# Kernel optimization log

Hardware: AMD Instinct MI355X
Metric: run time of the kernel (lower is better)

## Reference

```python
import jax, jax.numpy as jnp
import numpy as np


def conv1x1(x, w, b):
    # x: [B,Cin,H,W], w: [Cout,Cin], b: [Cout]
    return jnp.einsum('bchw,oc->bohw', x, w) + b[None, :, None, None]


def _lin_idx_w(in_size, out_size):
    # PyTorch bilinear, align_corners=False: src = max((i+0.5)*scale - 0.5, 0)
    scale = in_size / out_size
    src = jnp.maximum((jnp.arange(out_size, dtype=jnp.float32) + 0.5) * scale - 0.5, 0.0)
    i0 = jnp.floor(src).astype(jnp.int32)
    i0 = jnp.minimum(i0, in_size - 1)
    i1 = jnp.minimum(i0 + 1, in_size - 1)
    w1 = src - i0.astype(jnp.float32)
    return i0, i1, w1


def bilinear_resize(x, out_h, out_w):
    Hin, Win = x.shape[-2], x.shape[-1]
    y0, y1, wy = _lin_idx_w(Hin, out_h)
    x0, x1, wx = _lin_idx_w(Win, out_w)
    wy = wy[:, None]  # [out_h,1]
    rows = x[:, :, y0, :] * (1.0 - wy) + x[:, :, y1, :] * wy
    out = rows[:, :, :, x0] * (1.0 - wx) + rows[:, :, :, x1] * wx      # [B,C,out_h,out_w]
    return out


def setup_inputs() -> dict:
    key = jax.random.key(0)
    ks = jax.random.split(key, 10)
    C, C8 = 512, 64
    s = 1.0 / np.sqrt(C)
    return {
        'content': jax.random.normal(ks[0], (4, C, 64, 64), jnp.float32),
        'style': jax.random.normal(ks[1], (4, C, 80, 80), jnp.float32),
        'f_w': jax.random.normal(ks[2], (C8, C), jnp.float32) * s,
        'f_b': jax.random.normal(ks[3], (C8,), jnp.float32) * 0.01,
        'g_w': jax.random.normal(ks[4], (C8, C), jnp.float32) * s,
        'g_b': jax.random.normal(ks[5], (C8,), jnp.float32) * 0.01,
        'h_w': jax.random.normal(ks[6], (C, C), jnp.float32) * s,
        'h_b': jax.random.normal(ks[7], (C,), jnp.float32) * 0.01,
        'out_w': jax.random.normal(ks[8], (C, C), jnp.float32) * s,
        'out_b': jax.random.normal(ks[9], (C,), jnp.float32) * 0.01,
    }


def reference(content, style, f_w, f_b, g_w, g_b, h_w, h_b, out_w, out_b):
    B, C, H, W = content.shape
    HW = H * W
    f = conv1x1(content, f_w, f_b).reshape(B, -1, HW)                       # [B,C8,HW] (query, pre-transpose)
    g = bilinear_resize(conv1x1(style, g_w, g_b), H, W).reshape(B, -1, HW)  # [B,C8,HW]
    h = bilinear_resize(conv1x1(style, h_w, h_b), H, W).reshape(B, C, HW)   # [B,C,HW]
    attn = jax.nn.softmax(jnp.einsum('bcm,bcn->bmn', f, g), axis=-1)        # [B,HW_q,HW_k]
    out = jnp.einsum('bcn,bmn->bcm', h, attn).reshape(B, C, H, W)
    return conv1x1(out, out_w, out_b)
```

## Files before the change

### kernel.cpp

```cpp
#include <hip/hip_runtime.h>

#define NB 4
#define NC 512
#define ND 64
#define HW 4096
#define SPIN 6400

typedef _Float16 f16;
typedef _Float16 f16x8 __attribute__((ext_vector_type(8)));
typedef short s16x8 __attribute__((ext_vector_type(8)));
typedef float f32x4 __attribute__((ext_vector_type(4)));

__device__ __forceinline__ unsigned short f32_to_bf16(float x) {
  union { float f; unsigned u; } v; v.f = x;
  unsigned r = v.u + 0x7FFFu + ((v.u >> 16) & 1u);
  return (unsigned short)(r >> 16);
}

__device__ __forceinline__ void stv(float* p, float v) { *p = v; }
__device__ __forceinline__ void stv(f16* p, float v) { *p = (f16)v; }
__device__ __forceinline__ void stv(unsigned short* p, float v) { *p = f32_to_bf16(v); }

__global__ __launch_bounds__(256) void cvt_kernel(const float* __restrict__ in,
                                                  f16* __restrict__ out, int n) {
  int i = blockIdx.x * 256 + threadIdx.x;
  if (i < n) out[i] = (f16)in[i];
}

__global__ __launch_bounds__(256) void tcvt_kernel(const float* __restrict__ in,
                                                   f16* __restrict__ out) {
  __shared__ float Xs[64][65];
  int p0 = blockIdx.x * 64, c0 = blockIdx.y * 64, b = blockIdx.z;
  int t = threadIdx.x;
  const float* ib = in + ((size_t)b * NC + c0) * HW + p0;
  int pl = t & 63, cg = t >> 6;
#pragma unroll
  for (int k = 0; k < 16; ++k) {
    int c = cg * 16 + k;
    Xs[c][pl] = ib[(size_t)c * HW + pl];
  }
  __syncthreads();
  int p = t >> 2, cb = (t & 3) * 16;
  union { f16 h[16]; float4 q[2]; } u;
#pragma unroll
  for (int j = 0; j < 16; ++j) u.h[j] = (f16)Xs[cb + j][p];
  f16* ob = out + ((size_t)b * HW + p0 + p) * NC + c0 + cb;
  *(float4*)(ob) = u.q[0];
  *(float4*)(ob + 8) = u.q[1];
}

__global__ __launch_bounds__(256) void rstcvt_kernel(const float* __restrict__ X,
                                                     f16* __restrict__ Y) {
  __shared__ float Xs[64 * 165];
  int oy = blockIdx.x, c0 = blockIdx.y * 64, b = blockIdx.z;
  float syf = fmaxf((oy + 0.5f) * 1.25f - 0.5f, 0.f);
  int y0 = (int)syf; int y1 = min(y0 + 1, 79); float wy = syf - (float)y0;
  int t = threadIdx.x;
  const float* Xb = X + ((size_t)b * NC + c0) * SPIN;
#pragma unroll
  for (int k = 0; k < 10; ++k) {
    int idx = t + k * 256;
    int c = idx / 40;
    int rem = idx - c * 40;
    int yy = rem / 20;
    int x4 = rem - yy * 20;
    int ysrc = yy ? y1 : y0;
    float4 v = *(const float4*)(Xb + (size_t)c * SPIN + ysrc * 80 + x4 * 4);
    float* d = Xs + c * 165 + yy * 82 + x4 * 4;
    d[0] = v.x; d[1] = v.y; d[2] = v.z; d[3] = v.w;
  }
  __syncthreads();
  int ox = t >> 2, cb = (t & 3) * 16;
  float sxf = fmaxf((ox + 0.5f) * 1.25f - 0.5f, 0.f);
  int x0 = (int)sxf; int x1 = min(x0 + 1, 79); float wx = sxf - (float)x0;
  union { f16 h[16]; float4 q[2]; } u;
#pragma unroll
  for (int j = 0; j < 16; ++j) {
    const float* base = Xs + (cb + j) * 165;
    float a0 = base[x0], a1 = base[x1];
    float b0 = base[82 + x0], b1 = base[82 + x1];
    float r0 = a0 + (a1 - a0) * wx;
    float r1 = b0 + (b1 - b0) * wx;
    u.h[j] = (f16)(r0 + (r1 - r0) * wy);
  }
  f16* ob = Y + ((size_t)b * HW + oy * 64 + ox) * NC + c0 + cb;
  *(float4*)(ob) = u.q[0];
  *(float4*)(ob + 8) = u.q[1];
}

__global__ __launch_bounds__(256) void convpm_kernel(const f16* __restrict__ X,
                                                     const f16* __restrict__ W,
                                                     const float* __restrict__ bias,
                                                     f16* __restrict__ Y) {
  int b = blockIdx.z;
  int t = threadIdx.x, l = t & 63, w = t >> 6;
  int pw = blockIdx.x * 256 + w * 64;
  int l4 = l & 15, g = l >> 4;
  f32x4 acc[4][4] = {};
  const f16* Xb = X + ((size_t)b * HW + pw) * NC;
  for (int kk = 0; kk < 16; ++kk) {
    int co = kk * 32 + g * 8;
    f16x8 a[4], bb[4];
#pragma unroll
    for (int ms = 0; ms < 4; ++ms) a[ms] = *(const f16x8*)(Xb + (size_t)(ms * 16 + l4) * NC + co);
#pragma unroll
    for (int ct = 0; ct < 4; ++ct) bb[ct] = *(const f16x8*)(W + (size_t)(ct * 16 + l4) * NC + co);
#pragma unroll
    for (int ms = 0; ms < 4; ++ms)
#pragma unroll
      for (int ct = 0; ct < 4; ++ct)
        acc[ms][ct] = __builtin_amdgcn_mfma_f32_16x16x32_f16(a[ms], bb[ct], acc[ms][ct], 0, 0, 0);
  }
  float bv[4];
#pragma unroll
  for (int ct = 0; ct < 4; ++ct) bv[ct] = bias[ct * 16 + l4];
  f16* Yb = Y + ((size_t)b * HW + pw) * ND;
#pragma unroll
  for (int ms = 0; ms < 4; ++ms)
#pragma unroll
    for (int ct = 0; ct < 4; ++ct)
#pragma unroll
      for (int r = 0; r < 4; ++r)
        Yb[(size_t)(ms * 16 + g * 4 + r) * ND + ct * 16 + l4] = (f16)(acc[ms][ct][r] + bv[ct]);
}

template <typename OUT_T>
__global__ __launch_bounds__(256) void convcm_kernel(const f16* __restrict__ X,
                                                     const f16* __restrict__ W,
                                                     const float* __restrict__ bias,
                                                     OUT_T* __restrict__ Y, int O) {
  int b = blockIdx.z;
  int o0 = blockIdx.x * 64;
  int t = threadIdx.x, l = t & 63, w = t >> 6;
  int pw = blockIdx.y * 256 + w * 64;
  int l4 = l & 15, g = l >> 4;
  f32x4 acc[4][4] = {};
  const f16* Xb = X + ((size_t)b * HW + pw) * NC;
  const f16* Wb = W + (size_t)o0 * NC;
  for (int kk = 0; kk < 16; ++kk) {
    int co = kk * 32 + g * 8;
    f16x8 a[4], bb[4];
#pragma unroll
    for (int ms = 0; ms < 4; ++ms) a[ms] = *(const f16x8*)(Wb + (size_t)(ms * 16 + l4) * NC + co);
#pragma unroll
    for (int ct = 0; ct < 4; ++ct) bb[ct] = *(const f16x8*)(Xb + (size_t)(ct * 16 + l4) * NC + co);
#pragma unroll
    for (int ms = 0; ms < 4; ++ms)
#pragma unroll
      for (int ct = 0; ct < 4; ++ct)
        acc[ms][ct] = __builtin_amdgcn_mfma_f32_16x16x32_f16(a[ms], bb[ct], acc[ms][ct], 0, 0, 0);
  }
  float bv[4][4];
#pragma unroll
  for (int ms = 0; ms < 4; ++ms)
#pragma unroll
    for (int r = 0; r < 4; ++r) bv[ms][r] = bias[o0 + ms * 16 + g * 4 + r];
#pragma unroll
  for (int ms = 0; ms < 4; ++ms)
#pragma unroll
    for (int ct = 0; ct < 4; ++ct)
#pragma unroll
      for (int r = 0; r < 4; ++r) {
        float val = acc[ms][ct][r] + bv[ms][r];
        stv(&Y[((size_t)b * O + o0 + ms * 16 + g * 4 + r) * HW + pw + ct * 16 + l4], val);
      }
}

__global__ __launch_bounds__(512, 4) void attn_kernel(const f16* __restrict__ FT,
                                                      const f16* __restrict__ GT,
                                                      const unsigned short* __restrict__ HC,
                                                      f16* __restrict__ MIDT) {
  __shared__ __align__(16) char KsB[128 * 128];
  __shared__ __align__(16) char PsB[64 * 256];
  __shared__ float denP[8][16];
  int bid = blockIdx.x;
  int b = (bid & 7) >> 1;
  int cs = bid & 1;
  int m0 = (bid >> 3) * 64;
  int t = threadIdx.x, l = t & 63, w = t >> 6;
  int l4 = l & 15, g = l >> 4;
  int msq = w >> 1;
  int nsq = (w & 1) * 4;

  const f16* Fb = FT + ((size_t)b * HW + m0 + msq * 16 + l4) * ND + g * 8;
  f16x8 qa0 = *(const f16x8*)(Fb);
  f16x8 qa1 = *(const f16x8*)(Fb + 32);

  f32x4 acc[4][2] = {};
  float den_acc[4] = {0.f, 0.f, 0.f, 0.f};

  const f16* Gb = GT + (size_t)b * HW * ND;
  const unsigned short* Hb = HC + ((size_t)b * NC + cs * 256 + w * 32) * HW;

  for (int n0 = 0; n0 < HW; n0 += 128) {
    __syncthreads();
#pragma unroll
    for (int i = 0; i < 2; ++i) {
      int idx = t + i * 512;
      int nl = idx >> 3, cc = idx & 7;
      f16x8 kv = *(const f16x8*)(Gb + (size_t)(n0 + nl) * ND + cc * 8);
      *(f16x8*)(KsB + ((nl * 128 + cc * 16) ^ ((nl & 7) << 4))) = kv;
    }
    __syncthreads();
    float dp[4] = {0.f, 0.f, 0.f, 0.f};
#pragma unroll
    for (int f = 0; f < 4; ++f) {
      int n = (nsq + f) * 16 + l4;
      int sw = (n & 7) << 4;
      f16x8 kb0 = *(const f16x8*)(KsB + ((n * 128 + g * 16) ^ sw));
      f16x8 kb1 = *(const f16x8*)(KsB + ((n * 128 + 64 + g * 16) ^ sw));
      f32x4 s = {};
      s = __builtin_amdgcn_mfma_f32_16x16x32_f16(qa0, kb0, s, 0, 0, 0);
      s = __builtin_amdgcn_mfma_f32_16x16x32_f16(qa1, kb1, s, 0, 0, 0);
#pragma unroll
      for (int r = 0; r < 4; ++r) {
        float p = __expf(s[r]);
        dp[r] += p;
        int row = msq * 16 + g * 4 + r;
        *(unsigned short*)(PsB + ((row * 256 + n * 2) ^ ((row & 7) << 4))) = f32_to_bf16(p);
      }
    }
#pragma unroll
    for (int r = 0; r < 4; ++r) {
      float v = dp[r];
      v += __shfl_xor(v, 1); v += __shfl_xor(v, 2);
      v += __shfl_xor(v, 4); v += __shfl_xor(v, 8);
      den_acc[r] += v;
    }
    __syncthreads();
#pragma unroll
    for (int khh = 0; khh < 2; ++khh) {
      s16x8 pa[4][2];
#pragma unroll
      for (int ms = 0; ms < 4; ++ms) {
        int row = ms * 16 + l4;
        int sw = (row & 7) << 4;
        pa[ms][0] = *(const s16x8*)(PsB + ((row * 256 + khh * 128 + g * 16) ^ sw));
        pa[ms][1] = *(const s16x8*)(PsB + ((row * 256 + khh * 128 + 64 + g * 16) ^ sw));
      }
#pragma unroll
      for (int ct = 0; ct < 2; ++ct) {
        const unsigned short* hp = Hb + (size_t)(ct * 16 + l4) * HW + n0 + khh * 64 + g * 8;
        s16x8 vb0 = *(const s16x8*)(hp);
        s16x8 vb1 = *(const s16x8*)(hp + 32);
#pragma unroll
        for (int ms = 0; ms < 4; ++ms) {
          acc[ms][ct] = __builtin_amdgcn_mfma_f32_16x16x32_bf16(pa[ms][0], vb0, acc[ms][ct], 0, 0, 0);
          acc[ms][ct] = __builtin_amdgcn_mfma_f32_16x16x32_bf16(pa[ms][1], vb1, acc[ms][ct], 0, 0, 0);
        }
      }
    }
  }
  if (l4 == 0) {
#pragma unroll
    for (int r = 0; r < 4; ++r) denP[w][g * 4 + r] = den_acc[r];
  }
  __syncthreads();
  f16* Mb = MIDT + ((size_t)b * HW + m0) * NC + cs * 256 + w * 32;
#pragma unroll
  for (int ms = 0; ms < 4; ++ms)
#pragma unroll
    for (int r = 0; r < 4; ++r) {
      float rd = 1.f / (denP[2 * ms][g * 4 + r] + denP[2 * ms + 1][g * 4 + r]);
#pragma unroll
      for (int ct = 0; ct < 2; ++ct)
        Mb[(size_t)(ms * 16 + g * 4 + r) * NC + ct * 16 + l4] = (f16)(acc[ms][ct][r] * rd);
    }
}

extern "C" void kernel_launch(void* const* d_in, const int* in_sizes, int n_in,
                              void* d_out, int out_size, void* d_ws, size_t ws_size,
                              hipStream_t stream) {
  const float* content = (const float*)d_in[0];
  const float* style   = (const float*)d_in[1];
  const float* f_w = (const float*)d_in[2];
  const float* f_b = (const float*)d_in[3];
  const float* g_w = (const float*)d_in[4];
  const float* g_b = (const float*)d_in[5];
  const float* h_w = (const float*)d_in[6];
  const float* h_b = (const float*)d_in[7];
  const float* out_w = (const float*)d_in[8];
  const float* out_b = (const float*)d_in[9];
  float* out = (float*)d_out;

  const size_t MB = 1ull << 20;
  char* base = (char*)d_ws;
  f16* contentT = (f16*)base;
  f16* midT     = (f16*)base;
  unsigned short* hC = (unsigned short*)(base + 16 * MB);
  f16* fT = (f16*)(base + 32 * MB);
  f16* gT = (f16*)(base + 34 * MB);
  f16* styrT = (f16*)(base + 48 * MB);
  f16* fw16 = (f16*)(base + 64 * MB);
  f16* gw16 = fw16 + ND * NC;
  f16* hw16 = gw16 + ND * NC;
  f16* ow16 = hw16 + NC * NC;

  cvt_kernel<<<dim3((ND * NC + 255) / 256), 256, 0, stream>>>(f_w, fw16, ND * NC);
  cvt_kernel<<<dim3((ND * NC + 255) / 256), 256, 0, stream>>>(g_w, gw16, ND * NC);
  cvt_kernel<<<dim3((NC * NC + 255) / 256), 256, 0, stream>>>(h_w, hw16, NC * NC);
  cvt_kernel<<<dim3((NC * NC + 255) / 256), 256, 0, stream>>>(out_w, ow16, NC * NC);
  tcvt_kernel<<<dim3(HW / 64, NC / 64, NB), 256, 0, stream>>>(content, contentT);
  rstcvt_kernel<<<dim3(64, NC / 64, NB), 256, 0, stream>>>(style, styrT);
  convpm_kernel<<<dim3(HW / 256, 1, NB), 256, 0, stream>>>(contentT, fw16, f_b, fT);
  convpm_kernel<<<dim3(HW / 256, 1, NB), 256, 0, stream>>>(styrT, gw16, g_b, gT);
  convcm_kernel<unsigned short><<<dim3(NC / 64, HW / 256, NB), 256, 0, stream>>>(styrT, hw16, h_b, hC, NC);
  attn_kernel<<<dim3(512), 512, 0, stream>>>(fT, gT, hC, midT);
  convcm_kernel<float><<<dim3(NC / 64, HW / 256, NB), 256, 0, stream>>>(midT, ow16, out_b, out, NC);
}
```

Before: 318.1 us.

## Double-buffer key tiles in attention and merge small conversion/projection launches

The attention kernel now double-buffers the key tile in shared memory, prefetching the next tile into registers while computing the current one. It issues the V (h) global loads early, raises wave priority around the MFMA bursts and defers the denominator shuffle-reduction to after the loop. Separately, the four weight conversion launches are merged into one kernel and the f/g projections into one launch, cutting launch overhead. The changes add shared memory and register pressure in the attention kernel, which may lower occupancy.

```diff
diff --git a/kernel.cpp b/kernel.cpp
--- a/kernel.cpp
+++ b/kernel.cpp
@@ -21,10 +21,18 @@
 __device__ __forceinline__ void stv(f16* p, float v) { *p = (f16)v; }
 __device__ __forceinline__ void stv(unsigned short* p, float v) { *p = f32_to_bf16(v); }
 
-__global__ __launch_bounds__(256) void cvt_kernel(const float* __restrict__ in,
-                                                  f16* __restrict__ out, int n) {
+__global__ __launch_bounds__(256) void cvtw_kernel(const float* __restrict__ fw,
+                                                   const float* __restrict__ gw,
+                                                   const float* __restrict__ hw,
+                                                   const float* __restrict__ ow,
+                                                   f16* __restrict__ dst) {
   int i = blockIdx.x * 256 + threadIdx.x;
-  if (i < n) out[i] = (f16)in[i];
+  const float* src; int off;
+  if (i < 32768) { src = fw; off = 0; }
+  else if (i < 65536) { src = gw; off = 32768; }
+  else if (i < 327680) { src = hw; off = 65536; }
+  else { src = ow; off = 327680; }
+  dst[i] = (f16)src[i - off];
 }
 
 __global__ __launch_bounds__(256) void tcvt_kernel(const float* __restrict__ in,
@@ -88,11 +96,19 @@
   *(float4*)(ob + 8) = u.q[1];
 }
 
-__global__ __launch_bounds__(256) void convpm_kernel(const f16* __restrict__ X,
-                                                     const f16* __restrict__ W,
-                                                     const float* __restrict__ bias,
-                                                     f16* __restrict__ Y) {
-  int b = blockIdx.z;
+__global__ __launch_bounds__(256) void convpm2_kernel(const f16* __restrict__ X0,
+                                                      const f16* __restrict__ X1,
+                                                      const f16* __restrict__ W01,
+                                                      const float* __restrict__ b0,
+                                                      const float* __restrict__ b1,
+                                                      f16* __restrict__ Y0,
+                                                      f16* __restrict__ Y1) {
+  int sel = blockIdx.z >> 2;
+  int b = blockIdx.z & 3;
+  const f16* X = sel ? X1 : X0;
+  const f16* W = W01 + sel * (ND * NC);
+  const float* bias = sel ? b1 : b0;
+  f16* Y = sel ? Y1 : Y0;
   int t = threadIdx.x, l = t & 63, w = t >> 6;
   int pw = blockIdx.x * 256 + w * 64;
   int l4 = l & 15, g = l >> 4;
@@ -170,7 +186,7 @@
                                                       const f16* __restrict__ GT,
                                                       const unsigned short* __restrict__ HC,
                                                       f16* __restrict__ MIDT) {
-  __shared__ __align__(16) char KsB[128 * 128];
+  __shared__ __align__(16) char KsB[2][128 * 128];
   __shared__ __align__(16) char PsB[64 * 256];
   __shared__ float denP[8][16];
   int bid = blockIdx.x;
@@ -192,64 +208,99 @@
   const f16* Gb = GT + (size_t)b * HW * ND;
   const unsigned short* Hb = HC + ((size_t)b * NC + cs * 256 + w * 32) * HW;
 
-  for (int n0 = 0; n0 < HW; n0 += 128) {
-    __syncthreads();
-#pragma unroll
-    for (int i = 0; i < 2; ++i) {
-      int idx = t + i * 512;
-      int nl = idx >> 3, cc = idx & 7;
-      f16x8 kv = *(const f16x8*)(Gb + (size_t)(n0 + nl) * ND + cc * 8);
-      *(f16x8*)(KsB + ((nl * 128 + cc * 16) ^ ((nl & 7) << 4))) = kv;
-    }
-    __syncthreads();
-    float dp[4] = {0.f, 0.f, 0.f, 0.f};
+  int nl0 = t >> 3, cc0 = t & 7;
+  int ka0 = (nl0 * 128 + cc0 * 16) ^ ((nl0 & 7) << 4);
+  const f16* gsrc0 = Gb + (size_t)nl0 * ND + cc0 * 8;
+
+  const unsigned short* hb0 = Hb + (size_t)l4 * HW + g * 8;
+  const unsigned short* hb1 = Hb + (size_t)(16 + l4) * HW + g * 8;
+
+  {
+    f16x8 k0 = *(const f16x8*)(gsrc0);
+    f16x8 k1 = *(const f16x8*)(gsrc0 + (size_t)64 * ND);
+    *(f16x8*)(KsB[0] + ka0) = k0;
+    *(f16x8*)(KsB[0] + ka0 + 8192) = k1;
+  }
+  __syncthreads();
+
+  int cur = 0;
+  for (int it = 0; it < 32; ++it) {
+    int n0 = it * 128;
+    bool pre = (it < 31);
+    f16x8 k0, k1;
+    if (pre) {
+      const f16* gs = gsrc0 + (size_t)(n0 + 128) * ND;
+      k0 = *(const f16x8*)(gs);
+      k1 = *(const f16x8*)(gs + (size_t)64 * ND);
+    }
+    s16x8 vb00 = *(const s16x8*)(hb0 + n0);
+    s16x8 vb01 = *(const s16x8*)(hb0 + n0 + 32);
+    s16x8 vb10 = *(const s16x8*)(hb1 + n0);
+    s16x8 vb11 = *(const s16x8*)(hb1 + n0 + 32);
+
+    const char* Kc = KsB[cur];
 #pragma unroll
     for (int f = 0; f < 4; ++f) {
       int n = (nsq + f) * 16 + l4;
       int sw = (n & 7) << 4;
-      f16x8 kb0 = *(const f16x8*)(KsB + ((n * 128 + g * 16) ^ sw));
-      f16x8 kb1 = *(const f16x8*)(KsB + ((n * 128 + 64 + g * 16) ^ sw));
+      f16x8 kb0 = *(const f16x8*)(Kc + ((n * 128 + g * 16) ^ sw));
+      f16x8 kb1 = *(const f16x8*)(Kc + ((n * 128 + 64 + g * 16) ^ sw));
       f32x4 s = {};
       s = __builtin_amdgcn_mfma_f32_16x16x32_f16(qa0, kb0, s, 0, 0, 0);
       s = __builtin_amdgcn_mfma_f32_16x16x32_f16(qa1, kb1, s, 0, 0, 0);
 #pragma unroll
       for (int r = 0; r < 4; ++r) {
         float p = __expf(s[r]);
-        dp[r] += p;
+        den_acc[r] += p;
         int row = msq * 16 + g * 4 + r;
         *(unsigned short*)(PsB + ((row * 256 + n * 2) ^ ((row & 7) << 4))) = f32_to_bf16(p);
       }
     }
-#pragma unroll
-    for (int r = 0; r < 4; ++r) {
-      float v = dp[r];
-      v += __shfl_xor(v, 1); v += __shfl_xor(v, 2);
-      v += __shfl_xor(v, 4); v += __shfl_xor(v, 8);
-      den_acc[r] += v;
-    }
     __syncthreads();
+    if (pre) {
+      *(f16x8*)(KsB[cur ^ 1] + ka0) = k0;
+      *(f16x8*)(KsB[cur ^ 1] + ka0 + 8192) = k1;
+    }
+    s16x8 wb00 = *(const s16x8*)(hb0 + n0 + 64);
+    s16x8 wb01 = *(const s16x8*)(hb0 + n0 + 96);
+    s16x8 wb10 = *(const s16x8*)(hb1 + n0 + 64);
+    s16x8 wb11 = *(const s16x8*)(hb1 + n0 + 96);
 #pragma unroll
     for (int khh = 0; khh < 2; ++khh) {
-      s16x8 pa[4][2];
-#pragma unroll
-      for (int ms = 0; ms < 4; ++ms) {
-        int row = ms * 16 + l4;
-        int sw = (row & 7) << 4;
-        pa[ms][0] = *(const s16x8*)(PsB + ((row * 256 + khh * 128 + g * 16) ^ sw));
-        pa[ms][1] = *(const s16x8*)(PsB + ((row * 256 + khh * 128 + 64 + g * 16) ^ sw));
+      s16x8 v00 = khh ? wb00 : vb00, v01 = khh ? wb01 : vb01;
+      s16x8 v10 = khh ? wb10 : vb10, v11 = khh ? wb11 : vb11;
+#pragma unroll
+      for (int mh = 0; mh < 2; ++mh) {
+        s16x8 pa[2][2];
+#pragma unroll
+        for (int mi = 0; mi < 2; ++mi) {
+          int row = (mh * 2 + mi) * 16 + l4;
+          int sw = (row & 7) << 4;
+          pa[mi][0] = *(const s16x8*)(PsB + ((row * 256 + khh * 128 + g * 16) ^ sw));
+          pa[mi][1] = *(const s16x8*)(PsB + ((row * 256 + khh * 128 + 64 + g * 16) ^ sw));
+        }
+        __builtin_amdgcn_s_setprio(1);
+#pragma unroll
+        for (int mi = 0; mi < 2; ++mi) {
+          int ms = mh * 2 + mi;
+          acc[ms][0] = __builtin_amdgcn_mfma_f32_16x16x32_bf16(pa[mi][0], v00, acc[ms][0], 0, 0, 0);
+          acc[ms][0] = __builtin_amdgcn_mfma_f32_16x16x32_bf16(pa[mi][1], v01, acc[ms][0], 0, 0, 0);
+          acc[ms][1] = __builtin_amdgcn_mfma_f32_16x16x32_bf16(pa[mi][0], v10, acc[ms][1], 0, 0, 0);
+          acc[ms][1] = __builtin_amdgcn_mfma_f32_16x16x32_bf16(pa[mi][1], v11, acc[ms][1], 0, 0, 0);
+        }
+        __builtin_amdgcn_s_setprio(0);
       }
-#pragma unroll
-      for (int ct = 0; ct < 2; ++ct) {
-        const unsigned short* hp = Hb + (size_t)(ct * 16 + l4) * HW + n0 + khh * 64 + g * 8;
-        s16x8 vb0 = *(const s16x8*)(hp);
-        s16x8 vb1 = *(const s16x8*)(hp + 32);
-#pragma unroll
-        for (int ms = 0; ms < 4; ++ms) {
-          acc[ms][ct] = __builtin_amdgcn_mfma_f32_16x16x32_bf16(pa[ms][0], vb0, acc[ms][ct], 0, 0, 0);
-          acc[ms][ct] = __builtin_amdgcn_mfma_f32_16x16x32_bf16(pa[ms][1], vb1, acc[ms][ct], 0, 0, 0);
-        }
-      }
-    }
+    }
+    __syncthreads();
+    cur ^= 1;
+  }
+
+#pragma unroll
+  for (int r = 0; r < 4; ++r) {
+    float v = den_acc[r];
+    v += __shfl_xor(v, 1); v += __shfl_xor(v, 2);
+    v += __shfl_xor(v, 4); v += __shfl_xor(v, 8);
+    den_acc[r] = v;
   }
   if (l4 == 0) {
 #pragma unroll
@@ -291,19 +342,16 @@
   f16* fT = (f16*)(base + 32 * MB);
   f16* gT = (f16*)(base + 34 * MB);
   f16* styrT = (f16*)(base + 48 * MB);
-  f16* fw16 = (f16*)(base + 64 * MB);
-  f16* gw16 = fw16 + ND * NC;
-  f16* hw16 = gw16 + ND * NC;
-  f16* ow16 = hw16 + NC * NC;
-
-  cvt_kernel<<<dim3((ND * NC + 255) / 256), 256, 0, stream>>>(f_w, fw16, ND * NC);
-  cvt_kernel<<<dim3((ND * NC + 255) / 256), 256, 0, stream>>>(g_w, gw16, ND * NC);
-  cvt_kernel<<<dim3((NC * NC + 255) / 256), 256, 0, stream>>>(h_w, hw16, NC * NC);
-  cvt_kernel<<<dim3((NC * NC + 255) / 256), 256, 0, stream>>>(out_w, ow16, NC * NC);
+  f16* w16 = (f16*)(base + 64 * MB);
+  f16* fw16 = w16;
+  f16* gw16 = w16 + 32768;
+  f16* hw16 = w16 + 65536;
+  f16* ow16 = w16 + 327680;
+
+  cvtw_kernel<<<dim3(589824 / 256), 256, 0, stream>>>(f_w, g_w, h_w, out_w, w16);
   tcvt_kernel<<<dim3(HW / 64, NC / 64, NB), 256, 0, stream>>>(content, contentT);
   rstcvt_kernel<<<dim3(64, NC / 64, NB), 256, 0, stream>>>(style, styrT);
-  convpm_kernel<<<dim3(HW / 256, 1, NB), 256, 0, stream>>>(contentT, fw16, f_b, fT);
-  convpm_kernel<<<dim3(HW / 256, 1, NB), 256, 0, stream>>>(styrT, gw16, g_b, gT);
+  convpm2_kernel<<<dim3(HW / 256, 1, 2 * NB), 256, 0, stream>>>(contentT, styrT, fw16, f_b, g_b, fT, gT);
   convcm_kernel<unsigned short><<<dim3(NC / 64, HW / 256, NB), 256, 0, stream>>>(styrT, hw16, h_b, hC, NC);
   attn_kernel<<<dim3(512), 512, 0, stream>>>(fT, gT, hC, midT);
   convcm_kernel<float><<<dim3(NC / 64, HW / 256, NB), 256, 0, stream>>>(midT, ow16, out_b, out, NC);
```

Measured after the change: 291.7 us. -8.3%, faster.
